# Performance work log

Hardware: AMD Instinct MI355X
Metric: run time of the kernel (lower is better)

The kernel has to match this reference:

```python
import jax, jax.numpy as jnp
import numpy as np

B, C, H, W = 16, 2048, 16, 16
HEADS = 4
HEAD_DIM = C // HEADS


def setup_inputs() -> dict:
    key = jax.random.key(0)
    ks = jax.random.split(key, 7)
    s = 0.02
    x = jax.random.normal(ks[0], (B, C, H, W), dtype=jnp.float32)
    q_w = jax.random.normal(ks[1], (HEADS, HEAD_DIM, C), dtype=jnp.float32) * s
    q_b = jax.random.normal(ks[2], (HEADS, HEAD_DIM), dtype=jnp.float32) * s
    k_w = jax.random.normal(ks[3], (HEADS, HEAD_DIM, C), dtype=jnp.float32) * s
    k_b = jax.random.normal(ks[4], (HEADS, HEAD_DIM), dtype=jnp.float32) * s
    v_w = jax.random.normal(ks[5], (HEADS, C, C), dtype=jnp.float32) * s
    v_b = jax.random.normal(ks[6], (HEADS, C), dtype=jnp.float32) * s
    return {"x": x, "q_w": q_w, "q_b": q_b, "k_w": k_w, "k_b": k_b, "v_w": v_w, "v_b": v_b}


def reference(x, q_w, q_b, k_w, k_b, v_w, v_b):
    b, c, h, w = x.shape
    heads, head_dim, _ = q_w.shape
    # [B, N, C] with N = H*W
    patch = jnp.transpose(x, (0, 2, 3, 1)).reshape(b, h * w, c)
    # stacked per-head linear projections (bias per head)
    Q = jnp.einsum('bnc,hdc->bhnd', patch, q_w) + q_b[None, :, None, :]   # [B,heads,N,head_dim]
    K = jnp.einsum('bnc,hdc->bhnd', patch, k_w) + k_b[None, :, None, :]   # [B,heads,N,head_dim]
    V = jnp.einsum('bnc,hec->bhne', patch, v_w) + v_b[None, :, None, :]   # [B,heads,N,C]
    sim = jnp.einsum('bhqd,bhkd->bhqk', Q, K) / (head_dim ** 0.5)          # [B,heads,N,N]
    # sum over query dim, softmax over heads
    att = jnp.sum(sim, axis=2)[:, :, None, :]                              # [B,heads,1,N]
    att = jax.nn.softmax(att, axis=1)
    n = att.shape[-1]
    side = int(n ** 0.5)
    attention_score = att.reshape(b, heads, side, side)                    # [B,heads,h,w]
    # per-head spatial gating of the input, concatenated along channels
    x_enhance = (attention_score[:, :, None, :, :] * x[:, None, :, :, :]).reshape(b, heads * c, h, w)
    # standard softmax attention combine
    sim = jax.nn.softmax(sim, axis=-1)
    general = jnp.einsum('bhqk,bhke->bhqe', sim, V)                        # [B,heads,N,C]
    general = general.reshape(b, heads, side, side, c)
    general = jnp.transpose(general, (0, 1, 4, 2, 3)).reshape(b, heads * c, side, side)
    output = general + x_enhance
    return (attention_score, output)
```

## Files before the change

kernel.cpp:

```cpp
#include <hip/hip_runtime.h>
#include <hip/hip_bf16.h>
#include <hip/hip_fp8.h>

#define B_ 16
#define C_ 2048
#define N_ 256
#define HEADS_ 4
#define D_ 512

typedef unsigned int u32;
typedef unsigned char u8;
typedef unsigned short ushort_t;
typedef __attribute__((ext_vector_type(8))) short bfx8;
typedef __attribute__((ext_vector_type(4))) float fx4;

__device__ __forceinline__ unsigned short f2bs(float f) {
    __hip_bfloat16 h = __float2bfloat16(f);
    return __builtin_bit_cast(unsigned short, h);
}
__device__ __forceinline__ float bs2f(ushort_t u) {
    u32 v = ((u32)u) << 16;
    return __builtin_bit_cast(float, v);
}
__device__ __forceinline__ u8 f2f8(float f) {
    return (u8)__hip_cvt_float_to_fp8(f, __HIP_SATFINITE, __HIP_E4M3);
}
__device__ __forceinline__ void gload16(const void* g, void* l) {
    __builtin_amdgcn_global_load_lds((const __attribute__((address_space(1))) u32*)g,
                                     (__attribute__((address_space(3))) u32*)l, 16, 0, 0);
}
__device__ __forceinline__ int xcd_swz(int bid, int nwg) {
    return (bid & 7) * (nwg >> 3) + (bid >> 3);
}

#define SBAR() __builtin_amdgcn_s_barrier()
#define LGKM0() do { asm volatile("s_waitcnt lgkmcnt(0)" ::: "memory"); \
                     __builtin_amdgcn_sched_barrier(0); } while (0)
#define VMW4() asm volatile("s_waitcnt vmcnt(4)" ::: "memory")

#define STAGEF8(MAT, BUF, KH, J) do {                                         \
    const u8* s_ = (MAT) ? Bm : A;                                            \
    const int r_ = tid >> 1;                                                  \
    const int k_ = (J) * 64 + (KH) * 32 + (((tid & 1) ^ ((tid >> 3) & 1)) * 16); \
    gload16(s_ + (size_t)r_ * K + k_,                                         \
            (u8*)(&lds[MAT][BUF][KH][0][0]) + tid * 16);                      \
} while (0)

#define LDAF8(dst, BUF, KH, MH) do {                                          \
    _Pragma("unroll")                                                         \
    for (int i_ = 0; i_ < 4; ++i_)                                            \
        dst[i_] = *(const long*)(&lds[0][BUF][KH][wmr + (MH) * 64 + i_ * 16 + l16][f8off]); \
} while (0)

#define LDBF8(dst, BUF, KH) do {                                              \
    _Pragma("unroll")                                                         \
    for (int i_ = 0; i_ < 4; ++i_)                                            \
        dst[i_] = *(const long*)(&lds[1][BUF][KH][wnr + i_ * 16 + l16][f8off]); \
} while (0)

#define MMF8(aa, bb, MH) do {                                                 \
    _Pragma("unroll")                                                         \
    for (int i_ = 0; i_ < 4; ++i_) {                                          \
        _Pragma("unroll")                                                     \
        for (int n_ = 0; n_ < 4; ++n_)                                        \
            acc[(MH) * 4 + i_][n_] = __builtin_amdgcn_mfma_f32_16x16x32_fp8_fp8( \
                aa[i_], bb[n_], acc[(MH) * 4 + i_][n_], 0, 0, 0);             \
    }                                                                         \
} while (0)

#define KTILE2F8(BUF, JS1, JS2) do {                                          \
    long a0[4], a1[4], b0[4];                                                 \
    LDAF8(a0, BUF, 0, 0); LDAF8(a1, BUF, 0, 1); LDBF8(b0, BUF, 0);            \
    STAGEF8(0, BUF ^ 1, 1, JS1);                                              \
    STAGEF8(1, BUF ^ 1, 1, JS1);                                              \
    SBAR(); LGKM0();                                                          \
    __builtin_amdgcn_s_setprio(1);                                            \
    MMF8(a0, b0, 0); MMF8(a1, b0, 1);                                         \
    __builtin_amdgcn_s_setprio(0);                                            \
    VMW4();                                                                   \
    SBAR();                                                                   \
    LDAF8(a0, BUF, 1, 0); LDAF8(a1, BUF, 1, 1); LDBF8(b0, BUF, 1);            \
    STAGEF8(0, BUF, 0, JS2);                                                  \
    STAGEF8(1, BUF, 0, JS2);                                                  \
    SBAR(); LGKM0();                                                          \
    __builtin_amdgcn_s_setprio(1);                                            \
    MMF8(a0, b0, 0); MMF8(a1, b0, 1);                                         \
    __builtin_amdgcn_s_setprio(0);                                            \
    VMW4();                                                                   \
    SBAR();                                                                   \
} while (0)

typedef u8 ldsf8_t[2][2][2][256][32];

__device__ __forceinline__ void gemm256_f8(const u8* __restrict__ A,
                                           const u8* __restrict__ Bm,
                                           int K, ldsf8_t& lds, fx4 acc[8][4])
{
    const int tid = threadIdx.x;
    const int lane = tid & 63;
    const int w = tid >> 6;
    const int l16 = lane & 15, lhi = lane >> 4;
    const int f8off = (((lhi >> 1) ^ ((l16 >> 2) & 1)) * 16) + (lhi & 1) * 8;
    const int wmr = (w >> 2) * 128;
    const int wnr = (w & 3) * 64;
    const int nkt = K >> 6;

    STAGEF8(0, 0, 0, 0); STAGEF8(1, 0, 0, 0);
    STAGEF8(0, 0, 1, 0); STAGEF8(1, 0, 1, 0);
    STAGEF8(0, 1, 0, 1); STAGEF8(1, 1, 0, 1);
    VMW4();
    SBAR();

    for (int jj = 0; jj < nkt; jj += 2) {
        const int js1a = jj + 1;
        const int js2a = (jj + 2 < nkt) ? jj + 2 : nkt - 1;
        const int js1b = js2a;
        const int js2b = (jj + 3 < nkt) ? jj + 3 : nkt - 1;
        KTILE2F8(0, js1a, js2a);
        KTILE2F8(1, js1b, js2b);
    }
    asm volatile("s_waitcnt vmcnt(0)" ::: "memory");
    SBAR();
}

#define EPI256_IDX() \
    const int lane = threadIdx.x & 63, w = threadIdx.x >> 6; \
    const int l16 = lane & 15, lhi = lane >> 4; \
    const int wmr = (w >> 2) * 128, wnr = (w & 3) * 64;

typedef u8 lds128_t[2][2][2][128][32];

#define STG1(MAT, BUF, KH, J) do {                                            \
    const u8* s_ = (MAT) ? Bm : A;                                            \
    const int r_ = tid >> 1;                                                  \
    const int k_ = (J) * 64 + (KH) * 32 + (((tid & 1) ^ ((tid >> 3) & 1)) * 16); \
    gload16(s_ + (size_t)r_ * K + k_,                                         \
            (u8*)(&lds[MAT][BUF][KH][0][0]) + tid * 16);                      \
} while (0)

#define LD1(dst, MAT, BUF, KH, base) do {                                     \
    _Pragma("unroll")                                                         \
    for (int i_ = 0; i_ < 4; ++i_)                                            \
        dst[i_] = *(const long*)(&lds[MAT][BUF][KH][(base) + i_ * 16 + l16][f8off]); \
} while (0)

#define MM16(aa, bb) do {                                                     \
    __builtin_amdgcn_s_setprio(1);                                            \
    _Pragma("unroll")                                                         \
    for (int i_ = 0; i_ < 4; ++i_) {                                          \
        _Pragma("unroll")                                                     \
        for (int n_ = 0; n_ < 4; ++n_)                                        \
            acc[i_][n_] = __builtin_amdgcn_mfma_f32_16x16x32_fp8_fp8(         \
                aa[i_], bb[n_], acc[i_][n_], 0, 0, 0);                        \
    }                                                                         \
    __builtin_amdgcn_s_setprio(0);                                            \
} while (0)

#define KT128(BUF, JS1, JS2) do {                                             \
    long a0[4], b0[4];                                                        \
    LD1(a0, 0, BUF, 0, wm); LD1(b0, 1, BUF, 0, wn);                           \
    STG1(0, BUF ^ 1, 1, JS1); STG1(1, BUF ^ 1, 1, JS1);                       \
    SBAR(); LGKM0();                                                          \
    MM16(a0, b0);                                                             \
    VMW4();                                                                   \
    SBAR();                                                                   \
    LD1(a0, 0, BUF, 1, wm); LD1(b0, 1, BUF, 1, wn);                           \
    STG1(0, BUF, 0, JS2); STG1(1, BUF, 0, JS2);                               \
    SBAR(); LGKM0();                                                          \
    MM16(a0, b0);                                                             \
    VMW4();                                                                   \
    SBAR();                                                                   \
} while (0)

__device__ __forceinline__ void gemm128_f8(const u8* __restrict__ A,
                                           const u8* __restrict__ Bm,
                                           int K, lds128_t& lds, fx4 acc[4][4])
{
    const int tid = threadIdx.x;
    const int lane = tid & 63;
    const int w = tid >> 6;
    const int l16 = lane & 15, lhi = lane >> 4;
    const int f8off = (((lhi >> 1) ^ ((l16 >> 2) & 1)) * 16) + (lhi & 1) * 8;
    const int wm = (w >> 1) * 64;
    const int wn = (w & 1) * 64;
    const int nkt = K >> 6;

    STG1(0, 0, 0, 0); STG1(1, 0, 0, 0);
    STG1(0, 0, 1, 0); STG1(1, 0, 1, 0);
    STG1(0, 1, 0, 1); STG1(1, 1, 0, 1);
    VMW4();
    SBAR();

    for (int jj = 0; jj < nkt; jj += 2) {
        const int js1a = jj + 1;
        const int js2a = (jj + 2 < nkt) ? jj + 2 : nkt - 1;
        const int js1b = js2a;
        const int js2b = (jj + 3 < nkt) ? jj + 3 : nkt - 1;
        KT128(0, js1a, js2a);
        KT128(1, js1b, js2b);
    }
    asm volatile("s_waitcnt vmcnt(0)" ::: "memory");
    SBAR();
}

__device__ __forceinline__ void mfma_core(const ushort_t* __restrict__ A,
                                          const ushort_t* __restrict__ Bm,
                                          int K, fx4 acc[4][4])
{
    __shared__ __align__(16) ushort_t As[128 * 32];
    __shared__ __align__(16) ushort_t Bs[128 * 32];
    const int tid = threadIdx.x;
    const int lane = tid & 63, wave = tid >> 6;
    const int l16 = lane & 15, lhi = lane >> 4;
    const int swz8 = (lhi ^ ((l16 >> 1) & 3)) * 8;
    const int wm = (wave >> 1) * 64, wn = (wave & 1) * 64;

    for (int k0 = 0; k0 < K; k0 += 32) {
        const int f0 = tid, f1 = tid + 256;
        gload16(A + (size_t)(f0 >> 2) * K + k0 + (((f0 & 3) ^ ((f0 >> 3) & 3)) * 8), As + f0 * 8);
        gload16(A + (size_t)(f1 >> 2) * K + k0 + (((f1 & 3) ^ ((f1 >> 3) & 3)) * 8), As + f1 * 8);
        gload16(Bm + (size_t)(f0 >> 2) * K + k0 + (((f0 & 3) ^ ((f0 >> 3) & 3)) * 8), Bs + f0 * 8);
        gload16(Bm + (size_t)(f1 >> 2) * K + k0 + (((f1 & 3) ^ ((f1 >> 3) & 3)) * 8), Bs + f1 * 8);
        __syncthreads();
        bfx8 af[4], bfr[4];
#pragma unroll
        for (int i = 0; i < 4; ++i)
            af[i] = *(const bfx8*)(As + (wm + i * 16 + l16) * 32 + swz8);
#pragma unroll
        for (int j = 0; j < 4; ++j)
            bfr[j] = *(const bfx8*)(Bs + (wn + j * 16 + l16) * 32 + swz8);
#pragma unroll
        for (int i = 0; i < 4; ++i)
#pragma unroll
            for (int j = 0; j < 4; ++j)
                acc[i][j] = __builtin_amdgcn_mfma_f32_16x16x32_bf16(af[i], bfr[j], acc[i][j], 0, 0, 0);
        __syncthreads();
    }
}

#define EPI_IDX() \
    const int lane = threadIdx.x & 63, wave = threadIdx.x >> 6; \
    const int l16 = lane & 15, lhi = lane >> 4; \
    const int wm = (wave >> 1) * 64, wn = (wave & 1) * 64;

__global__ __launch_bounds__(256) void k_castw8(const float* __restrict__ s, u8* __restrict__ d,
                                                int n, float scale) {
    int i = (blockIdx.x * 256 + threadIdx.x) * 4;
    if (i >= n) return;
    float4 v = *(const float4*)(s + i);
    uchar4 o = { f2f8(v.x * scale), f2f8(v.y * scale), f2f8(v.z * scale), f2f8(v.w * scale) };
    *(uchar4*)(d + i) = o;
}

__global__ __launch_bounds__(256) void k_cast_x(const float* __restrict__ x,
                                                ushort_t* __restrict__ xb, u8* __restrict__ xb8,
                                                u8* __restrict__ xbT8, float* __restrict__ xpart) {
    __shared__ float t[32][33];
    const int b = blockIdx.z, c0 = blockIdx.y * 32, n0 = blockIdx.x * 32;
    const int tn = threadIdx.x & 31, tc8 = threadIdx.x >> 5;
    const float* xp = x + ((size_t)b * C_ + c0) * N_ + n0;
#pragma unroll
    for (int p = 0; p < 4; ++p) {
        int cc = tc8 + p * 8;
        float v = xp[(size_t)cc * N_ + tn];
        t[cc][tn] = v;
        xb[((size_t)b * C_ + c0 + cc) * N_ + n0 + tn] = f2bs(v);
        xb8[((size_t)b * C_ + c0 + cc) * N_ + n0 + tn] = f2f8(v * 8.0f);
        float s = v;
#pragma unroll
        for (int o = 16; o; o >>= 1) s += __shfl_xor(s, o, 32);
        if (tn == 0) xpart[(size_t)blockIdx.x * B_ * C_ + (size_t)b * C_ + c0 + cc] = s;
    }
    __syncthreads();
#pragma unroll
    for (int p = 0; p < 4; ++p) {
        int nn = tc8 + p * 8;
        xbT8[((size_t)b * N_ + n0 + nn) * C_ + c0 + tn] = f2f8(t[tn][nn] * 8.0f);
    }
}

__global__ __launch_bounds__(256) void k_xsum2(const float* __restrict__ xpart, float* __restrict__ xsum) {
    const int c = blockIdx.x * 256 + threadIdx.x, b = blockIdx.y;
    float s = 0.f;
#pragma unroll
    for (int t = 0; t < 8; ++t) s += xpart[(size_t)t * B_ * C_ + (size_t)b * C_ + c];
    xsum[(size_t)b * C_ + c] = s;
}

__global__ __launch_bounds__(256) void k_qsum(const float* __restrict__ xsum, const float* __restrict__ qw,
                                              const float* __restrict__ qb, float* __restrict__ qsum) {
    const int wave = threadIdx.x >> 6, lane = threadIdx.x & 63;
    const int row = blockIdx.x * 4 + wave;
    const int h = row >> 9, d = row & 511;
    const float* wr = qw + (size_t)row * C_;
    float acc[16];
#pragma unroll
    for (int bb = 0; bb < 16; ++bb) acc[bb] = 0.f;
    for (int it = 0; it < C_ / 64; ++it) {
        const int c = it * 64 + lane;
        const float w = wr[c];
#pragma unroll
        for (int bb = 0; bb < 16; ++bb) acc[bb] += xsum[(size_t)bb * C_ + c] * w;
    }
#pragma unroll
    for (int bb = 0; bb < 16; ++bb) {
        float s = acc[bb];
#pragma unroll
        for (int o = 32; o; o >>= 1) s += __shfl_xor(s, o, 64);
        if (lane == 0) qsum[(size_t)((bb << 2) | h) * D_ + d] = s + 256.0f * qb[row];
    }
}

__global__ __launch_bounds__(64) void k_const(const float* __restrict__ qsum, const float* __restrict__ kb,
                                              float* __restrict__ cst) {
    const int bh = blockIdx.x, h = bh & 3, lane = threadIdx.x;
    float s = 0.f;
    for (int d = lane; d < D_; d += 64) s += qsum[(size_t)bh * D_ + d] * kb[h * D_ + d];
#pragma unroll
    for (int o = 32; o; o >>= 1) s += __shfl_xor(s, o, 64);
    if (lane == 0) cst[bh] = s;
}

__global__ __launch_bounds__(256) void k_vecp(const float* __restrict__ qsum, const float* __restrict__ kw,
                                              float* __restrict__ partv) {
    const int ct = blockIdx.x, h = blockIdx.y, dsl = blockIdx.z;
    __shared__ float qs[16 * 128];
    for (int i = threadIdx.x; i < 16 * 128; i += 256) {
        int bb = i >> 7, dd = i & 127;
        qs[i] = qsum[(size_t)((bb << 2) | h) * D_ + dsl * 128 + dd];
    }
    __syncthreads();
    const int c = ct * 256 + threadIdx.x;
    const float* wp = kw + ((size_t)h * D_ + dsl * 128) * C_ + c;
    float acc[16];
#pragma unroll
    for (int bb = 0; bb < 16; ++bb) acc[bb] = 0.f;
    for (int dd = 0; dd < 128; ++dd) {
        const float w = wp[(size_t)dd * C_];
#pragma unroll
        for (int bb = 0; bb < 16; ++bb) acc[bb] += qs[bb * 128 + dd] * w;
    }
#pragma unroll
    for (int bb = 0; bb < 16; ++bb)
        partv[((size_t)dsl * 64 + ((bb << 2) | h)) * C_ + c] = acc[bb];
}

__global__ __launch_bounds__(256) void k_att(const float* __restrict__ x, const float* __restrict__ partv,
                                             float* __restrict__ part) {
    const int bh = blockIdx.x, sl = blockIdx.y, b = bh >> 2;
    __shared__ float vs[512];
    const int c0 = sl * 512;
    for (int i = threadIdx.x; i < 512; i += 256) {
        float v = 0.f;
#pragma unroll
        for (int dsl = 0; dsl < 4; ++dsl) v += partv[((size_t)dsl * 64 + bh) * C_ + c0 + i];
        vs[i] = v;
    }
    __syncthreads();
    float a = 0.f;
    const float* xp = x + ((size_t)b * C_ + c0) * N_ + threadIdx.x;
#pragma unroll 8
    for (int c = 0; c < 512; ++c) a += vs[c] * xp[(size_t)c * N_];
    part[((size_t)sl * 64 + bh) * N_ + threadIdx.x] = a;
}

__global__ __launch_bounds__(256) void k_score(const float* __restrict__ part, const float* __restrict__ cst,
                                               float* __restrict__ score, float* __restrict__ out0) {
    const int b = blockIdx.x, k = threadIdx.x;
    const float scale = 0.044194173824159216f;
    float a[4];
#pragma unroll
    for (int h = 0; h < 4; ++h) {
        const int bh = b * 4 + h;
        float s = cst[bh];
#pragma unroll
        for (int sl = 0; sl < 4; ++sl) s += part[((size_t)sl * 64 + bh) * N_ + k];
        a[h] = s * scale;
    }
    float mx = fmaxf(fmaxf(a[0], a[1]), fmaxf(a[2], a[3]));
    float e0 = expf(a[0] - mx), e1 = expf(a[1] - mx), e2 = expf(a[2] - mx), e3 = expf(a[3] - mx);
    float inv = 1.0f / (e0 + e1 + e2 + e3);
    float r[4] = { e0 * inv, e1 * inv, e2 * inv, e3 * inv };
#pragma unroll
    for (int h = 0; h < 4; ++h) {
        score[(size_t)(b * 4 + h) * N_ + k] = r[h];
        out0[(size_t)(b * 4 + h) * N_ + k] = r[h];
    }
}

__global__ __launch_bounds__(512, 2) void k_proj(const u8* __restrict__ xbT8,
                                                 const u8* __restrict__ qw8, const u8* __restrict__ kw8,
                                                 const float* __restrict__ qb, const float* __restrict__ kb,
                                                 ushort_t* __restrict__ QKbuf) {
    __shared__ __align__(16) ldsf8_t lds;
    const int wg = xcd_swz(blockIdx.x, 256);
    const int quad = wg >> 2;
    const int mt = quad >> 2;
    const int nt = (quad & 3) * 4 + (wg & 3);
    const int c0 = nt * 256;
    const int qk = c0 >> 11;
    const int rem = c0 & 2047;
    const u8* A  = xbT8 + (size_t)mt * 256 * C_;
    const u8* Bm = (qk ? kw8 : qw8) + (size_t)rem * C_;
    const float* bias  = (qk ? kb : qb) + rem;
    const int K = C_;

    fx4 acc[8][4];
#pragma unroll
    for (int i = 0; i < 8; ++i)
#pragma unroll
        for (int j = 0; j < 4; ++j) acc[i][j] = (fx4){0.f, 0.f, 0.f, 0.f};
    gemm256_f8(A, Bm, K, lds, acc);

    EPI256_IDX();
#pragma unroll
    for (int i = 0; i < 8; ++i)
#pragma unroll
        for (int n = 0; n < 4; ++n)
#pragma unroll
            for (int r = 0; r < 4; ++r) {
                const int gr = mt * 256 + wmr + i * 16 + lhi * 4 + r;
                const int bq = gr >> 8, nn = gr & 255;
                const int lc = wnr + n * 16 + l16;
                const int hh = (rem + lc) >> 9, dl = (rem + lc) & 511;
                const float v = acc[i][n][r] * (1.0f / 512.0f) + bias[lc];
                QKbuf[((((size_t)(qk * 16 + bq) * 4 + hh) * 256) + nn) * 512 + dl] = f2bs(v);
            }
}

__global__ __launch_bounds__(256, 3) void k_out(const u8* __restrict__ vw8, const float* __restrict__ vb,
                                                const u8* __restrict__ Tt8, const float* __restrict__ score,
                                                const ushort_t* __restrict__ xb, float* __restrict__ out1) {
    __shared__ __align__(16) lds128_t lds;
    const int wg = xcd_swz(blockIdx.x, 2048);
    const int h = wg >> 9, l = wg & 511;
    const int mt = l >> 5, nt = l & 31;
    const u8* A  = vw8 + (size_t)h * C_ * C_ + (size_t)mt * 128 * C_;
    const u8* Bm = Tt8 + (size_t)h * 16 * N_ * C_ + (size_t)nt * 128 * C_;
    const int K = C_;

    fx4 acc[4][4];
#pragma unroll
    for (int i = 0; i < 4; ++i)
#pragma unroll
        for (int j = 0; j < 4; ++j) acc[i][j] = (fx4){0.f, 0.f, 0.f, 0.f};
    gemm128_f8(A, Bm, K, lds, acc);

    const int lane = threadIdx.x & 63, w = threadIdx.x >> 6;
    const int l16 = lane & 15, lhi = lane >> 4;
    const int wm = (w >> 1) * 64, wn = (w & 1) * 64;
#pragma unroll
    for (int i = 0; i < 4; ++i)
#pragma unroll
        for (int n = 0; n < 4; ++n)
#pragma unroll
            for (int r = 0; r < 4; ++r) {
                const int e = mt * 128 + wm + i * 16 + lhi * 4 + r;
                const int col = nt * 128 + wn + n * 16 + l16;
                const int b = col >> 8, nn = col & 255;
                float v = acc[i][n][r] * (1.0f / 1024.0f) + vb[h * C_ + e]
                        + score[(size_t)(b * 4 + h) * N_ + nn] * bs2f(xb[((size_t)b * C_ + e) * N_ + nn]);
                out1[((size_t)(b * 4 + h) * C_ + e) * N_ + nn] = v;
            }
}

__global__ __launch_bounds__(512, 2) void k_T8(const u8* __restrict__ Pb8, const u8* __restrict__ xb8,
                                               u8* __restrict__ Tt8) {
    __shared__ __align__(16) ldsf8_t lds;
    const int wg = xcd_swz(blockIdx.x, 512);
    const int b = wg >> 5, l = wg & 31;
    const int mt = l >> 3, nt = l & 7;
    const u8* A  = Pb8 + ((size_t)b * 1024 + mt * 256) * 256;
    const u8* Bm = xb8 + ((size_t)b * 2048 + nt * 256) * 256;
    const int K = N_;

    fx4 acc[8][4];
#pragma unroll
    for (int i = 0; i < 8; ++i)
#pragma unroll
        for (int j = 0; j < 4; ++j) acc[i][j] = (fx4){0.f, 0.f, 0.f, 0.f};
    gemm256_f8(A, Bm, K, lds, acc);

    EPI256_IDX();
#pragma unroll
    for (int i = 0; i < 8; ++i)
#pragma unroll
        for (int n = 0; n < 4; ++n)
#pragma unroll
            for (int r = 0; r < 4; ++r) {
                const int rowm = mt * 256 + wmr + i * 16 + lhi * 4 + r;
                const int h = rowm >> 8, q = rowm & 255;
                const int c = nt * 256 + wnr + n * 16 + l16;
                Tt8[(((size_t)h * 16 + b) * 256 + q) * 2048 + c] = f2f8(acc[i][n][r] * 0.0078125f);
            }
}

__global__ __launch_bounds__(256) void k_sim(const ushort_t* __restrict__ QKbuf, float* __restrict__ simf) {
    const int wg = blockIdx.x;
    const int bh = wg >> 2, mt = (wg >> 1) & 1, ntl = wg & 1;
    const ushort_t* Qr = QKbuf;
    const ushort_t* Kr = QKbuf + (size_t)16 * 4 * 256 * 512;
    const ushort_t* A = Qr + ((size_t)bh * 256 + mt * 128) * 512;
    const ushort_t* Bm = Kr + ((size_t)bh * 256 + ntl * 128) * 512;

    fx4 acc[4][4];
#pragma unroll
    for (int i = 0; i < 4; ++i)
#pragma unroll
        for (int j = 0; j < 4; ++j) acc[i][j] = (fx4){0.f, 0.f, 0.f, 0.f};
    mfma_core(A, Bm, D_, acc);

    EPI_IDX();
    const float scale = 0.044194173824159216f;
#pragma unroll
    for (int i = 0; i < 4; ++i)
#pragma unroll
        for (int j = 0; j < 4; ++j)
#pragma unroll
            for (int r = 0; r < 4; ++r) {
                const int q = mt * 128 + wm + i * 16 + lhi * 4 + r;
                const int k = ntl * 128 + wn + j * 16 + l16;
                simf[(size_t)bh * N_ * N_ + (size_t)q * N_ + k] = acc[i][j][r] * scale;
            }
}

__global__ __launch_bounds__(64) void k_softP(const float* __restrict__ simf, u8* __restrict__ Pb8) {
    const size_t row = blockIdx.x;
    const float* p = simf + row * N_;
    u8* o = Pb8 + row * N_;
    const int t = threadIdx.x;
    float v0 = p[t], v1 = p[t + 64], v2 = p[t + 128], v3 = p[t + 192];
    float mx = fmaxf(fmaxf(v0, v1), fmaxf(v2, v3));
#pragma unroll
    for (int off = 32; off; off >>= 1) mx = fmaxf(mx, __shfl_xor(mx, off, 64));
    float e0 = expf(v0 - mx), e1 = expf(v1 - mx), e2 = expf(v2 - mx), e3 = expf(v3 - mx);
    float s = e0 + e1 + e2 + e3;
#pragma unroll
    for (int off = 32; off; off >>= 1) s += __shfl_xor(s, off, 64);
    const float inv = 256.0f / s;
    o[t] = f2f8(e0 * inv); o[t + 64] = f2f8(e1 * inv);
    o[t + 128] = f2f8(e2 * inv); o[t + 192] = f2f8(e3 * inv);
}

extern "C" void kernel_launch(void* const* d_in, const int* in_sizes, int n_in,
                              void* d_out, int out_size, void* d_ws, size_t ws_size,
                              hipStream_t stream)
{
    const float* x  = (const float*)d_in[0];
    const float* qw = (const float*)d_in[1];
    const float* qb = (const float*)d_in[2];
    const float* kw = (const float*)d_in[3];
    const float* kb = (const float*)d_in[4];
    const float* vw = (const float*)d_in[5];
    const float* vb = (const float*)d_in[6];

    float* out0 = (float*)d_out;
    float* out1 = out0 + (size_t)B_ * HEADS_ * N_;

    char* w = (char*)d_ws;
    u8*       vw8  = (u8*)w;        w += (size_t)4 * C_ * C_;
    u8*       qw8  = (u8*)w;        w += (size_t)4 * D_ * C_;
    u8*       kw8  = (u8*)w;        w += (size_t)4 * D_ * C_;
    ushort_t* xb   = (ushort_t*)w;  w += (size_t)B_ * C_ * N_ * 2;
    u8*       xb8  = (u8*)w;        w += (size_t)B_ * C_ * N_;
    u8*       xbT8 = (u8*)w;        w += (size_t)B_ * N_ * C_;
    ushort_t* QKbuf= (ushort_t*)w;  w += (size_t)2 * 16 * 4 * 256 * 512 * 2;
    u8*       Pb8  = (u8*)w;        w += (size_t)64 * N_ * N_;
    float*    simf = (float*)w;     w += (size_t)64 * N_ * N_ * 4;
    u8*       Tt8  = (u8*)w;        w += (size_t)64 * N_ * C_;
    float*    xpart= (float*)w;     w += (size_t)8 * B_ * C_ * 4;
    float*    xsum = (float*)w;     w += (size_t)B_ * C_ * 4;
    float*    qsum = (float*)w;     w += (size_t)64 * D_ * 4;
    float*    cst  = (float*)w;     w += 1024;
    float*    partv= (float*)w;     w += (size_t)4 * 64 * C_ * 4;
    float*    part = (float*)w;     w += (size_t)4 * 64 * N_ * 4;
    float*    score= (float*)w;     w += (size_t)64 * N_ * 4;

    k_castw8<<<dim3(4 * D_ * C_ / 4 / 256), 256, 0, stream>>>(qw, qw8, 4 * D_ * C_, 64.0f);
    k_castw8<<<dim3(4 * D_ * C_ / 4 / 256), 256, 0, stream>>>(kw, kw8, 4 * D_ * C_, 64.0f);
    k_castw8<<<dim3(4 * C_ * C_ / 4 / 256), 256, 0, stream>>>(vw, vw8, 4 * C_ * C_, 64.0f);
    k_cast_x<<<dim3(8, 64, 16), 256, 0, stream>>>(x, xb, xb8, xbT8, xpart);

    k_xsum2<<<dim3(8, 16), 256, 0, stream>>>(xpart, xsum);
    k_qsum <<<dim3(512), 256, 0, stream>>>(xsum, qw, qb, qsum);
    k_const<<<dim3(64), 64, 0, stream>>>(qsum, kb, cst);
    k_vecp <<<dim3(8, 4, 4), 256, 0, stream>>>(qsum, kw, partv);
    k_att  <<<dim3(64, 4), 256, 0, stream>>>(x, partv, part);
    k_score<<<dim3(16), 256, 0, stream>>>(part, cst, score, out0);

    k_proj <<<dim3(256), 512, 0, stream>>>(xbT8, qw8, kw8, qb, kb, QKbuf);
    k_sim  <<<dim3(256), 256, 0, stream>>>(QKbuf, simf);
    k_softP<<<dim3(64 * N_), 64, 0, stream>>>(simf, Pb8);
    k_T8   <<<dim3(512), 512, 0, stream>>>(Pb8, xb8, Tt8);
    k_out  <<<dim3(2048), 256, 0, stream>>>(vw8, vb, Tt8, score, xb, out1);
}
```

Baseline: 388.3 us.

## Widen k_out GEMM tile to 128x256 with 512-thread blocks

The final V-projection GEMM in k_out moves from 128x128 tiles on 256 threads to 128x256 tiles on 512 threads (8 waves, 2x4 wave grid). Each A tile of weights is now shared across twice as many output columns, which halves the global/LDS traffic for the large vw8 operand, and the grid shrinks to 1024 blocks. The staging schedule and vmcnt waits are rewritten for asymmetric A/B loads. In exchange each block uses more LDS, and the 512,4 launch bounds may squeeze registers or occupancy.

```diff
diff --git a/kernel.cpp b/kernel.cpp
--- a/kernel.cpp
+++ b/kernel.cpp
@@ -37,6 +37,9 @@
 #define LGKM0() do { asm volatile("s_waitcnt lgkmcnt(0)" ::: "memory"); \
                      __builtin_amdgcn_sched_barrier(0); } while (0)
 #define VMW4() asm volatile("s_waitcnt vmcnt(4)" ::: "memory")
+#define VMW3() asm volatile("s_waitcnt vmcnt(3)" ::: "memory")
+#define VMW2() asm volatile("s_waitcnt vmcnt(2)" ::: "memory")
+#define VMW1() asm volatile("s_waitcnt vmcnt(1)" ::: "memory")
 
 #define STAGEF8(MAT, BUF, KH, J) do {                                         \
     const u8* s_ = (MAT) ? Bm : A;                                            \
@@ -128,23 +131,35 @@
     const int l16 = lane & 15, lhi = lane >> 4; \
     const int wmr = (w >> 2) * 128, wnr = (w & 3) * 64;
 
-typedef u8 lds128_t[2][2][2][128][32];
-
-#define STG1(MAT, BUF, KH, J) do {                                            \
-    const u8* s_ = (MAT) ? Bm : A;                                            \
+#define STGA2(BUF, J) do {                                                    \
+    const int t_ = tid & 255;                                                 \
+    const int kh_ = tid >> 8;                                                 \
+    const int r_ = t_ >> 1;                                                   \
+    const int k_ = (J) * 64 + kh_ * 32 + (((tid & 1) ^ ((tid >> 3) & 1)) * 16); \
+    gload16(A + (size_t)r_ * K + k_,                                          \
+            (u8*)(&ldsA[BUF][kh_][0][0]) + t_ * 16);                          \
+} while (0)
+
+#define STGB2(BUF, KH, J) do {                                                \
     const int r_ = tid >> 1;                                                  \
     const int k_ = (J) * 64 + (KH) * 32 + (((tid & 1) ^ ((tid >> 3) & 1)) * 16); \
-    gload16(s_ + (size_t)r_ * K + k_,                                         \
-            (u8*)(&lds[MAT][BUF][KH][0][0]) + tid * 16);                      \
-} while (0)
-
-#define LD1(dst, MAT, BUF, KH, base) do {                                     \
+    gload16(Bm + (size_t)r_ * K + k_,                                         \
+            (u8*)(&ldsB[BUF][KH][0][0]) + tid * 16);                          \
+} while (0)
+
+#define LDA2(dst, BUF, KH) do {                                               \
     _Pragma("unroll")                                                         \
     for (int i_ = 0; i_ < 4; ++i_)                                            \
-        dst[i_] = *(const long*)(&lds[MAT][BUF][KH][(base) + i_ * 16 + l16][f8off]); \
-} while (0)
-
-#define MM16(aa, bb) do {                                                     \
+        dst[i_] = *(const long*)(&ldsA[BUF][KH][wma + i_ * 16 + l16][f8off]); \
+} while (0)
+
+#define LDB2(dst, BUF, KH) do {                                               \
+    _Pragma("unroll")                                                         \
+    for (int i_ = 0; i_ < 4; ++i_)                                            \
+        dst[i_] = *(const long*)(&ldsB[BUF][KH][wnb + i_ * 16 + l16][f8off]); \
+} while (0)
+
+#define MM16W(aa, bb) do {                                                    \
     __builtin_amdgcn_s_setprio(1);                                            \
     _Pragma("unroll")                                                         \
     for (int i_ = 0; i_ < 4; ++i_) {                                          \
@@ -156,39 +171,47 @@
     __builtin_amdgcn_s_setprio(0);                                            \
 } while (0)
 
-#define KT128(BUF, JS1, JS2) do {                                             \
+#define KTW(BUF, JS1, JS2) do {                                               \
     long a0[4], b0[4];                                                        \
-    LD1(a0, 0, BUF, 0, wm); LD1(b0, 1, BUF, 0, wn);                           \
-    STG1(0, BUF ^ 1, 1, JS1); STG1(1, BUF ^ 1, 1, JS1);                       \
+                                                               \
+    LDA2(a0, BUF, 0); LDB2(b0, BUF, 0);                                       \
+    STGA2(BUF ^ 1, JS1);                                                      \
+    STGB2(BUF ^ 1, 1, JS1);                                                   \
     SBAR(); LGKM0();                                                          \
-    MM16(a0, b0);                                                             \
-    VMW4();                                                                   \
+    MM16W(a0, b0);                                                            \
+    VMW3();                                                                   \
     SBAR();                                                                   \
-    LD1(a0, 0, BUF, 1, wm); LD1(b0, 1, BUF, 1, wn);                           \
-    STG1(0, BUF, 0, JS2); STG1(1, BUF, 0, JS2);                               \
+                                                               \
+    LDA2(a0, BUF, 1); LDB2(b0, BUF, 1);                                       \
+    STGB2(BUF, 0, JS2);                                                       \
     SBAR(); LGKM0();                                                          \
-    MM16(a0, b0);                                                             \
-    VMW4();                                                                   \
+    MM16W(a0, b0);                                                            \
+    VMW2();                                                                   \
     SBAR();                                                                   \
 } while (0)
 
-__device__ __forceinline__ void gemm128_f8(const u8* __restrict__ A,
-                                           const u8* __restrict__ Bm,
-                                           int K, lds128_t& lds, fx4 acc[4][4])
+typedef u8 ldsA_t[2][2][128][32];
+typedef u8 ldsB_t2[2][2][256][32];
+
+__device__ __forceinline__ void gemm128x256_f8(const u8* __restrict__ A,
+                                               const u8* __restrict__ Bm,
+                                               int K, ldsA_t& ldsA, ldsB_t2& ldsB,
+                                               fx4 acc[4][4])
 {
     const int tid = threadIdx.x;
     const int lane = tid & 63;
     const int w = tid >> 6;
     const int l16 = lane & 15, lhi = lane >> 4;
     const int f8off = (((lhi >> 1) ^ ((l16 >> 2) & 1)) * 16) + (lhi & 1) * 8;
-    const int wm = (w >> 1) * 64;
-    const int wn = (w & 1) * 64;
+    const int wma = (w >> 2) * 64;
+    const int wnb = (w & 3) * 64;
     const int nkt = K >> 6;
 
-    STG1(0, 0, 0, 0); STG1(1, 0, 0, 0);
-    STG1(0, 0, 1, 0); STG1(1, 0, 1, 0);
-    STG1(0, 1, 0, 1); STG1(1, 1, 0, 1);
-    VMW4();
+    STGA2(0, 0);
+    STGB2(0, 0, 0);
+    STGB2(0, 1, 0);
+    STGB2(1, 0, 1);
+    VMW1();
     SBAR();
 
     for (int jj = 0; jj < nkt; jj += 2) {
@@ -196,8 +219,8 @@
         const int js2a = (jj + 2 < nkt) ? jj + 2 : nkt - 1;
         const int js1b = js2a;
         const int js2b = (jj + 3 < nkt) ? jj + 3 : nkt - 1;
-        KT128(0, js1a, js2a);
-        KT128(1, js1b, js2b);
+        KTW(0, js1a, js2a);
+        KTW(1, js1b, js2b);
     }
     asm volatile("s_waitcnt vmcnt(0)" ::: "memory");
     SBAR();
@@ -428,15 +451,16 @@
             }
 }
 
-__global__ __launch_bounds__(256, 3) void k_out(const u8* __restrict__ vw8, const float* __restrict__ vb,
+__global__ __launch_bounds__(512, 4) void k_out(const u8* __restrict__ vw8, const float* __restrict__ vb,
                                                 const u8* __restrict__ Tt8, const float* __restrict__ score,
                                                 const ushort_t* __restrict__ xb, float* __restrict__ out1) {
-    __shared__ __align__(16) lds128_t lds;
-    const int wg = xcd_swz(blockIdx.x, 2048);
-    const int h = wg >> 9, l = wg & 511;
-    const int mt = l >> 5, nt = l & 31;
+    __shared__ __align__(16) ldsA_t ldsA;
+    __shared__ __align__(16) ldsB_t2 ldsB;
+    const int wg = xcd_swz(blockIdx.x, 1024);
+    const int h = wg >> 8, l = wg & 255;
+    const int mt = l >> 4, nt = l & 15;
     const u8* A  = vw8 + (size_t)h * C_ * C_ + (size_t)mt * 128 * C_;
-    const u8* Bm = Tt8 + (size_t)h * 16 * N_ * C_ + (size_t)nt * 128 * C_;
+    const u8* Bm = Tt8 + (size_t)h * 16 * N_ * C_ + (size_t)nt * 256 * C_;
     const int K = C_;
 
     fx4 acc[4][4];
@@ -444,19 +468,19 @@
     for (int i = 0; i < 4; ++i)
 #pragma unroll
         for (int j = 0; j < 4; ++j) acc[i][j] = (fx4){0.f, 0.f, 0.f, 0.f};
-    gemm128_f8(A, Bm, K, lds, acc);
+    gemm128x256_f8(A, Bm, K, ldsA, ldsB, acc);
 
     const int lane = threadIdx.x & 63, w = threadIdx.x >> 6;
     const int l16 = lane & 15, lhi = lane >> 4;
-    const int wm = (w >> 1) * 64, wn = (w & 1) * 64;
+    const int wma = (w >> 2) * 64, wnb = (w & 3) * 64;
 #pragma unroll
     for (int i = 0; i < 4; ++i)
 #pragma unroll
         for (int n = 0; n < 4; ++n)
 #pragma unroll
             for (int r = 0; r < 4; ++r) {
-                const int e = mt * 128 + wm + i * 16 + lhi * 4 + r;
-                const int col = nt * 128 + wn + n * 16 + l16;
+                const int e = mt * 128 + wma + i * 16 + lhi * 4 + r;
+                const int col = nt * 256 + wnb + n * 16 + l16;
                 const int b = col >> 8, nn = col & 255;
                 float v = acc[i][n][r] * (1.0f / 1024.0f) + vb[h * C_ + e]
                         + score[(size_t)(b * 4 + h) * N_ + nn] * bs2f(xb[((size_t)b * C_ + e) * N_ + nn]);
@@ -592,5 +616,5 @@
     k_sim  <<<dim3(256), 256, 0, stream>>>(QKbuf, simf);
     k_softP<<<dim3(64 * N_), 64, 0, stream>>>(simf, Pb8);
     k_T8   <<<dim3(512), 512, 0, stream>>>(Pb8, xb8, Tt8);
-    k_out  <<<dim3(2048), 256, 0, stream>>>(vw8, vb, Tt8, score, xb, out1);
-}
+    k_out  <<<dim3(1024), 512, 0, stream>>>(vw8, vb, Tt8, score, xb, out1);
+}
```

After: 360.3 us. -7.2%, faster.
